# Optimization experiments

Measured on AMD Instinct MI355X. Metric: run time of the kernel, lower is better.

The kernel has to match this reference:

```python
import jax, jax.numpy as jnp
import numpy as np

EPS = 1e-7  # keras.backend.epsilon()
ROUTINGS = 3


def squash(v, axis=-1):
    # scale = ||v||^2 / (1+||v||^2) / sqrt(||v||^2 + eps)
    s2 = jnp.sum(jnp.square(v), axis=axis, keepdims=True)
    return v * (s2 / (1.0 + s2) / jnp.sqrt(s2 + EPS))


def setup_inputs() -> dict:
    key = jax.random.key(0)
    k1, k2 = jax.random.split(key)
    B, I, P = 256, 1152, 8   # batch, primcap_num, primcap_dim
    J, D = 10, 16            # digitcap_num, digitcap_dim
    x = jax.random.normal(k1, (B, I, P), dtype=jnp.float32)
    W = jax.random.normal(k2, (I, J, D, P), dtype=jnp.float32) * 0.01
    return {"x": x, "W": W}


def reference(x, W):
    # votes u_hat[b,i,j,d] = W[i,j,d,:] @ x[b,i,:]  (implicit broadcast, no tiling)
    votes = jnp.einsum('ijdp,bip->bijd', W, x)            # [B,I,J,D]
    B, I, J, _ = votes.shape
    b = jnp.zeros((B, I, J), dtype=votes.dtype)
    v = None
    for r in range(ROUTINGS):
        c = jax.nn.softmax(b, axis=2)                      # over digit capsules
        s = jnp.einsum('bij,bijd->bjd', c, votes)          # weighted sum over prim caps
        v = squash(s, axis=-1)                             # [B,J,D]
        if r < ROUTINGS - 1:
            b = b + jnp.einsum('bijd,bjd->bij', votes, v)  # agreement
    return v
```

## Files before the change

kernel.cpp:

```cpp
#include <hip/hip_runtime.h>
#include <cstdint>
#include <cstddef>

constexpr int Bn = 256, In = 1152, Pn = 8, Jn = 10, Dn = 16;
constexpr int CA = 8, NCH = In / CA;
constexpr int PADX = 18;

typedef float v2f __attribute__((ext_vector_type(2)));

template <int CTRL>
__device__ __forceinline__ float dpp_add(float v) {
  const int s =
      __builtin_amdgcn_update_dpp(0, __float_as_int(v), CTRL, 0xf, 0xf, true);
  return v + __int_as_float(s);
}

__device__ __forceinline__ float rowsum16(float v) {
  v = dpp_add<0xB1>(v);
  v = dpp_add<0x4E>(v);
  v = dpp_add<0x124>(v);
  v = dpp_add<0x128>(v);
  return v;
}

__device__ __forceinline__ v2f pkdot8(const float4 w0, const float4 w1,
                                      const float4 x0, const float4 x1) {
  v2f wa, wb, wc, wd, xa, xb, xc, xd;
  wa.x = w0.x; wa.y = w0.y; wb.x = w0.z; wb.y = w0.w;
  wc.x = w1.x; wc.y = w1.y; wd.x = w1.z; wd.y = w1.w;
  xa.x = x0.x; xa.y = x0.y; xb.x = x0.z; xb.y = x0.w;
  xc.x = x1.x; xc.y = x1.y; xd.x = x1.z; xd.y = x1.w;
  v2f acc = wa * xa;
  acc = __builtin_elementwise_fma(wb, xb, acc);
  acc = __builtin_elementwise_fma(wc, xc, acc);
  acc = __builtin_elementwise_fma(wd, xd, acc);
  return acc;
}

template <int MODE>
__global__ __launch_bounds__(256)
__attribute__((amdgpu_waves_per_eu(3, 4)))
void capsV(const float* __restrict__ x, const float* __restrict__ w,
           const float* __restrict__ vsumT, float* __restrict__ spart) {
  __shared__ float4 wlds[CA * Jn * 2 * 16];
  __shared__ float4 xlds[32 * PADX];
  const int t = threadIdx.x;
  const int d = t & 15, q = t >> 4;
  const int ch = blockIdx.x;
  const int bbase = blockIdx.y * 32;
  const int b0 = bbase + q, b1 = b0 + 16;
  const int i0 = ch * CA;

  {
    const float4* wg =
        reinterpret_cast<const float4*>(w + (size_t)i0 * (Jn * Dn * Pn));
    for (int k = 0; k < 10; ++k) {
      const int g = t + k * 256;
      const int h = g & 1, dd = (g >> 1) & 15, ij = g >> 5;
      wlds[(ij * 2 + h) * 16 + dd] = wg[g];
    }
  }
  {
    for (int k = 0; k < 2; ++k) {
      const int u = t + k * 256;
      const int bl = u >> 4, idx = u & 15;
      xlds[bl * PADX + idx] = reinterpret_cast<const float4*>(
          x + ((size_t)(bbase + bl) * In + i0) * Pn)[idx];
    }
  }

  v2f vs2[Jn], acc2[Jn];
  #pragma unroll
  for (int j = 0; j < Jn; ++j) {
    acc2[j] = (v2f)(0.f);
    if (MODE) {
      vs2[j].x = vsumT[((size_t)j * Bn + b0) * Dn + d];
      vs2[j].y = vsumT[((size_t)j * Bn + b1) * Dn + d];
    }
  }

  __syncthreads();

  for (int ii = 0; ii < CA; ++ii) {
    const float4 xa0 = xlds[q * PADX + ii * 2];
    const float4 xa1 = xlds[q * PADX + ii * 2 + 1];
    const float4 xb0 = xlds[(q + 16) * PADX + ii * 2];
    const float4 xb1 = xlds[(q + 16) * PADX + ii * 2 + 1];

    v2f vt2[Jn];
    #pragma unroll
    for (int j = 0; j < Jn; ++j) {
      const float4* wrow = &wlds[((ii * Jn + j) * 2) * 16 + d];
      const float4 w0 = wrow[0];
      const float4 w1 = wrow[16];
      const v2f pa = pkdot8(w0, w1, xa0, xa1);
      const v2f pb = pkdot8(w0, w1, xb0, xb1);
      vt2[j].x = pa.x + pa.y;
      vt2[j].y = pb.x + pb.y;
    }

    if (MODE) {
      v2f e2[Jn], sum2 = (v2f)(0.f);
      #pragma unroll
      for (int j = 0; j < Jn; ++j) {
        const v2f lp = vt2[j] * vs2[j];
        e2[j].x = __expf(rowsum16(lp.x));
        e2[j].y = __expf(rowsum16(lp.y));
        sum2 += e2[j];
      }
      v2f inv2;
      inv2.x = __builtin_amdgcn_rcpf(sum2.x);
      inv2.y = __builtin_amdgcn_rcpf(sum2.y);
      #pragma unroll
      for (int j = 0; j < Jn; ++j)
        acc2[j] = __builtin_elementwise_fma(e2[j] * inv2, vt2[j], acc2[j]);
    } else {
      #pragma unroll
      for (int j = 0; j < Jn; ++j) acc2[j] += vt2[j];
    }
  }

  const float cs = MODE ? 1.f : 0.1f;
  #pragma unroll
  for (int j = 0; j < Jn; ++j) {
    spart[(((size_t)ch * Jn + j) * Bn + b0) * Dn + d] = acc2[j].x * cs;
    spart[(((size_t)ch * Jn + j) * Bn + b1) * Dn + d] = acc2[j].y * cs;
  }
}

template <int MODE>
__global__ __launch_bounds__(1024) void capsF(
    const float* __restrict__ spart, float* __restrict__ vsumT,
    float* __restrict__ out) {
  __shared__ float red[8][8][16];
  const int t = threadIdx.x;
  const int cg = t >> 7, r = t & 127, g = r >> 4, d = r & 15;
  const int j = blockIdx.x, b = blockIdx.y * 8 + g;

  const size_t cstride = (size_t)Jn * Bn * Dn;
  const size_t cstep = 8 * cstride;
  const float* sp = spart + (((size_t)cg * Jn + j) * Bn + b) * Dn + d;
  float s0 = 0.f, s1 = 0.f;
  #pragma unroll 3
  for (int k = 0; k < NCH / 8; k += 2) {
    s0 += sp[0];
    s1 += sp[cstep];
    sp += 2 * cstep;
  }
  red[cg][g][d] = s0 + s1;
  __syncthreads();
  if (t < 128) {
    float z = 0.f;
    #pragma unroll
    for (int c = 0; c < 8; ++c) z += red[c][g][d];
    const float n2 = rowsum16(z * z);
    const float sc = n2 / (1.f + n2) / sqrtf(n2 + 1e-7f);
    const float v = z * sc;
    if (MODE == 2) {
      out[((size_t)b * Jn + j) * Dn + d] = v;
    } else if (MODE == 1) {
      vsumT[((size_t)j * Bn + b) * Dn + d] += v;
    } else {
      vsumT[((size_t)j * Bn + b) * Dn + d] = v;
    }
  }
}

extern "C" void kernel_launch(void* const* d_in, const int* in_sizes, int n_in,
                              void* d_out, int out_size, void* d_ws, size_t ws_size,
                              hipStream_t stream) {
  const float* x = (const float*)d_in[0];
  const float* w = (const float*)d_in[1];
  float* vsumT = (float*)d_ws;
  float* spart = vsumT + (size_t)Jn * Bn * Dn;
  float* out = (float*)d_out;

  const dim3 gV(NCH, Bn / 32), gF(Jn, Bn / 8);

  capsV<0><<<gV, 256, 0, stream>>>(x, w, nullptr, spart);
  capsF<0><<<gF, 1024, 0, stream>>>(spart, vsumT, out);

  capsV<1><<<gV, 256, 0, stream>>>(x, w, vsumT, spart);
  capsF<1><<<gF, 1024, 0, stream>>>(spart, vsumT, out);

  capsV<1><<<gV, 256, 0, stream>>>(x, w, vsumT, spart);
  capsF<2><<<gF, 1024, 0, stream>>>(spart, vsumT, out);
}
```

Baseline: 155.9 us.

## Materialize votes once and reuse them in later routing passes

Splits the vote kernel into one that computes votes, writes them to a global workspace buffer and forms the first-iteration partial sums, and a routing kernel that reads the stored votes instead of recomputing them from W and x. This removes the repeated dot-product work in the second and third routing passes. In exchange it adds a very large global write and two full reads of the vote tensor, turning compute-bound passes into memory-bound ones, and it requires a much larger workspace.

```diff
diff --git a/kernel.cpp b/kernel.cpp
--- a/kernel.cpp
+++ b/kernel.cpp
@@ -37,11 +37,10 @@
   return acc;
 }
 
-template <int MODE>
 __global__ __launch_bounds__(256)
 __attribute__((amdgpu_waves_per_eu(3, 4)))
-void capsV(const float* __restrict__ x, const float* __restrict__ w,
-           const float* __restrict__ vsumT, float* __restrict__ spart) {
+void capsVW(const float* __restrict__ x, const float* __restrict__ w,
+            float* __restrict__ votes, float* __restrict__ spart) {
   __shared__ float4 wlds[CA * Jn * 2 * 16];
   __shared__ float4 xlds[32 * PADX];
   const int t = threadIdx.x;
@@ -69,15 +68,9 @@
     }
   }
 
-  v2f vs2[Jn], acc2[Jn];
-  #pragma unroll
-  for (int j = 0; j < Jn; ++j) {
-    acc2[j] = (v2f)(0.f);
-    if (MODE) {
-      vs2[j].x = vsumT[((size_t)j * Bn + b0) * Dn + d];
-      vs2[j].y = vsumT[((size_t)j * Bn + b1) * Dn + d];
-    }
-  }
+  v2f acc2[Jn];
+  #pragma unroll
+  for (int j = 0; j < Jn; ++j) acc2[j] = (v2f)(0.f);
 
   __syncthreads();
 
@@ -87,7 +80,7 @@
     const float4 xb0 = xlds[(q + 16) * PADX + ii * 2];
     const float4 xb1 = xlds[(q + 16) * PADX + ii * 2 + 1];
 
-    v2f vt2[Jn];
+    float* vrow = votes + ((size_t)(i0 + ii) * Jn) * (Bn * Dn) + d;
     #pragma unroll
     for (int j = 0; j < Jn; ++j) {
       const float4* wrow = &wlds[((ii * Jn + j) * 2) * 16 + d];
@@ -95,36 +88,71 @@
       const float4 w1 = wrow[16];
       const v2f pa = pkdot8(w0, w1, xa0, xa1);
       const v2f pb = pkdot8(w0, w1, xb0, xb1);
-      vt2[j].x = pa.x + pa.y;
-      vt2[j].y = pb.x + pb.y;
-    }
-
-    if (MODE) {
-      v2f e2[Jn], sum2 = (v2f)(0.f);
-      #pragma unroll
-      for (int j = 0; j < Jn; ++j) {
-        const v2f lp = vt2[j] * vs2[j];
-        e2[j].x = __expf(rowsum16(lp.x));
-        e2[j].y = __expf(rowsum16(lp.y));
-        sum2 += e2[j];
-      }
-      v2f inv2;
-      inv2.x = __builtin_amdgcn_rcpf(sum2.x);
-      inv2.y = __builtin_amdgcn_rcpf(sum2.y);
-      #pragma unroll
-      for (int j = 0; j < Jn; ++j)
-        acc2[j] = __builtin_elementwise_fma(e2[j] * inv2, vt2[j], acc2[j]);
-    } else {
-      #pragma unroll
-      for (int j = 0; j < Jn; ++j) acc2[j] += vt2[j];
-    }
-  }
-
-  const float cs = MODE ? 1.f : 0.1f;
+      v2f vt;
+      vt.x = pa.x + pa.y;
+      vt.y = pb.x + pb.y;
+      vrow[(size_t)j * (Bn * Dn) + b0 * Dn] = vt.x;
+      vrow[(size_t)j * (Bn * Dn) + b1 * Dn] = vt.y;
+      acc2[j] += vt;
+    }
+  }
+
   #pragma unroll
   for (int j = 0; j < Jn; ++j) {
-    spart[(((size_t)ch * Jn + j) * Bn + b0) * Dn + d] = acc2[j].x * cs;
-    spart[(((size_t)ch * Jn + j) * Bn + b1) * Dn + d] = acc2[j].y * cs;
+    spart[(((size_t)ch * Jn + j) * Bn + b0) * Dn + d] = acc2[j].x * 0.1f;
+    spart[(((size_t)ch * Jn + j) * Bn + b1) * Dn + d] = acc2[j].y * 0.1f;
+  }
+}
+
+__global__ __launch_bounds__(256)
+__attribute__((amdgpu_waves_per_eu(3, 4)))
+void capsR(const float* __restrict__ votes, const float* __restrict__ vsumT,
+           float* __restrict__ spart) {
+  const int t = threadIdx.x;
+  const int d = t & 15, q = t >> 4;
+  const int ch = blockIdx.x;
+  const int bbase = blockIdx.y * 32;
+  const int b0 = bbase + q, b1 = b0 + 16;
+  const int i0 = ch * CA;
+
+  v2f vs2[Jn], acc2[Jn];
+  #pragma unroll
+  for (int j = 0; j < Jn; ++j) {
+    acc2[j] = (v2f)(0.f);
+    vs2[j].x = vsumT[((size_t)j * Bn + b0) * Dn + d];
+    vs2[j].y = vsumT[((size_t)j * Bn + b1) * Dn + d];
+  }
+
+  for (int ii = 0; ii < CA; ++ii) {
+    const float* vrow = votes + ((size_t)(i0 + ii) * Jn) * (Bn * Dn) + d;
+
+    v2f vt2[Jn];
+    #pragma unroll
+    for (int j = 0; j < Jn; ++j) {
+      vt2[j].x = vrow[(size_t)j * (Bn * Dn) + b0 * Dn];
+      vt2[j].y = vrow[(size_t)j * (Bn * Dn) + b1 * Dn];
+    }
+
+    v2f e2[Jn], sum2 = (v2f)(0.f);
+    #pragma unroll
+    for (int j = 0; j < Jn; ++j) {
+      const v2f lp = vt2[j] * vs2[j];
+      e2[j].x = __expf(rowsum16(lp.x));
+      e2[j].y = __expf(rowsum16(lp.y));
+      sum2 += e2[j];
+    }
+    v2f inv2;
+    inv2.x = __builtin_amdgcn_rcpf(sum2.x);
+    inv2.y = __builtin_amdgcn_rcpf(sum2.y);
+    #pragma unroll
+    for (int j = 0; j < Jn; ++j)
+      acc2[j] = __builtin_elementwise_fma(e2[j] * inv2, vt2[j], acc2[j]);
+  }
+
+  #pragma unroll
+  for (int j = 0; j < Jn; ++j) {
+    spart[(((size_t)ch * Jn + j) * Bn + b0) * Dn + d] = acc2[j].x;
+    spart[(((size_t)ch * Jn + j) * Bn + b1) * Dn + d] = acc2[j].y;
   }
 }
 
@@ -173,16 +201,17 @@
   const float* w = (const float*)d_in[1];
   float* vsumT = (float*)d_ws;
   float* spart = vsumT + (size_t)Jn * Bn * Dn;
+  float* votes = spart + (size_t)NCH * Jn * Bn * Dn;
   float* out = (float*)d_out;
 
   const dim3 gV(NCH, Bn / 32), gF(Jn, Bn / 8);
 
-  capsV<0><<<gV, 256, 0, stream>>>(x, w, nullptr, spart);
+  capsVW<<<gV, 256, 0, stream>>>(x, w, votes, spart);
   capsF<0><<<gF, 1024, 0, stream>>>(spart, vsumT, out);
 
-  capsV<1><<<gV, 256, 0, stream>>>(x, w, vsumT, spart);
+  capsR<<<gV, 256, 0, stream>>>(votes, vsumT, spart);
   capsF<1><<<gF, 1024, 0, stream>>>(spart, vsumT, out);
 
-  capsV<1><<<gV, 256, 0, stream>>>(x, w, vsumT, spart);
+  capsR<<<gV, 256, 0, stream>>>(votes, vsumT, spart);
   capsF<2><<<gF, 1024, 0, stream>>>(spart, vsumT, out);
 }
```

Measured after the change: 185.4 us. 18.9% more time.
